# Kernel optimization log

Hardware: AMD Instinct MI355X
Metric: run time of the kernel (lower is better)

## Reference

```python
import jax, jax.numpy as jnp
import numpy as np

N, K, M = 1024, 256, 1024
INIT_SCALE = 0.1


def setup_inputs() -> dict:
    key = jax.random.key(0)
    kx, kw = jax.random.split(key)
    x = jax.random.normal(kx, (N, K), dtype=jnp.float32)
    weight = jax.random.normal(kw, (M, K), dtype=jnp.float32) * INIT_SCALE
    return {"x": x, "weight": weight}


def reference(x, weight):
    # Tropical (max-plus) matmul: out[n, m] = max_k(|x[n, k]| + |w[m, k]|)
    ax = jnp.abs(x)        # [N, K]
    aw = jnp.abs(weight)   # [M, K]
    # broadcast to [N, M, K] then reduce over K (mirrors the original expand+add+max)
    return jnp.max(ax[:, None, :] + aw[None, :, :], axis=2)  # [N, M]
```

## Files before the change

kernel.cpp:

```cpp
#include <hip/hip_runtime.h>


typedef float v2f __attribute__((ext_vector_type(2)));
typedef float v4f __attribute__((ext_vector_type(4)));

constexpr int K    = 256;
constexpr int N    = 1024;
constexpr int M    = 1024;
constexpr int TILE = 64;
constexpr int KH   = 128;
constexpr int KPL  = KH / 2;

__global__ void __launch_bounds__(256, 2)
tropical_main(const float* __restrict__ xg, const float* __restrict__ wg,
              float* __restrict__ pw)
{
    __shared__ __align__(16) v2f xs[KPL * 64];
    __shared__ __align__(16) v2f wsh[KPL * 64];

    const int tid = threadIdx.x;
    const int tx  = tid & 15;
    const int ty  = tid >> 4;
    const int bt  = (int)blockIdx.x & 255;
    const int kh  = (int)blockIdx.x >> 8;
    const int bn  = (bt >> 4) * TILE;
    const int bm  = (bt & 15) * TILE;
    const int k0  = kh * KH;

    const int r0 = tid >> 3;
    const int l  = tid & 7;
    const v4f* x0 = (const v4f*)(xg + (bn + r0     ) * K + k0);
    const v4f* x1 = (const v4f*)(xg + (bn + r0 + 32) * K + k0);
    const v4f* w0 = (const v4f*)(wg + (bm + r0     ) * K + k0);
    const v4f* w1 = (const v4f*)(wg + (bm + r0 + 32) * K + k0);

#pragma unroll
    for (int i = 0; i < 4; ++i) {
        const int q   = l + 8 * i;
        const int kpl = 2 * q;
        v4f a = x0[q];
        v4f b = x1[q];
        v4f c = w0[q];
        v4f d = w1[q];
        const int s0 = ((kpl    ) & 3) << 2;
        const int s1 = ((kpl + 1) & 3) << 2;
        xs [(kpl    ) * 64 + ((r0     ) ^ s0)] = (v2f){fabsf(a.x), fabsf(a.y)};
        xs [(kpl + 1) * 64 + ((r0     ) ^ s1)] = (v2f){fabsf(a.z), fabsf(a.w)};
        xs [(kpl    ) * 64 + ((r0 + 32) ^ s0)] = (v2f){fabsf(b.x), fabsf(b.y)};
        xs [(kpl + 1) * 64 + ((r0 + 32) ^ s1)] = (v2f){fabsf(b.z), fabsf(b.w)};
        wsh[(kpl    ) * 64 + ((r0     ) ^ s0)] = (v2f){fabsf(c.x), fabsf(c.y)};
        wsh[(kpl + 1) * 64 + ((r0     ) ^ s1)] = (v2f){fabsf(c.z), fabsf(c.w)};
        wsh[(kpl    ) * 64 + ((r0 + 32) ^ s0)] = (v2f){fabsf(d.x), fabsf(d.y)};
        wsh[(kpl + 1) * 64 + ((r0 + 32) ^ s1)] = (v2f){fabsf(d.z), fabsf(d.w)};
    }

    __syncthreads();

    float acc[4][4];
#pragma unroll
    for (int a2 = 0; a2 < 4; ++a2)
#pragma unroll
        for (int b2 = 0; b2 < 4; ++b2) acc[a2][b2] = 0.f;

    const int ty0 = ty;        const int tx0 = tx;
    const int ty4 = ty ^ 4;    const int tx4 = tx ^ 4;
    const int ty8 = ty ^ 8;    const int tx8 = tx ^ 8;
    const int ty12 = ty ^ 12;  const int tx12 = tx ^ 12;

#define PHASE(J, TYJ, TXJ)                                                   \
    do {                                                                     \
        const v2f* xr = xs  + (kp4 + (J)) * 64;                              \
        const v2f* wr = wsh + (kp4 + (J)) * 64;                              \
        v2f xa[4] = {xr[(TYJ)], xr[(TYJ) + 16], xr[(TYJ) + 32], xr[(TYJ) + 48]}; \
        v2f wa[4] = {wr[(TXJ)], wr[(TXJ) + 16], wr[(TXJ) + 32], wr[(TXJ) + 48]}; \
        _Pragma("unroll")                                                    \
        for (int a2 = 0; a2 < 4; ++a2)                                       \
            _Pragma("unroll")                                                \
            for (int b2 = 0; b2 < 4; ++b2) {                                 \
                v2f s = xa[a2] + wa[b2];                   \
                acc[a2][b2] = fmaxf(acc[a2][b2], fmaxf(s.x, s.y)); \
            }                                                                \
    } while (0)

    for (int kp4 = 0; kp4 < KPL; kp4 += 4) {
        PHASE(0, ty0,  tx0);
        PHASE(1, ty4,  tx4);
        PHASE(2, ty8,  tx8);
        PHASE(3, ty12, tx12);
    }
#undef PHASE

    float* slab = pw + kh * (N * M);
#pragma unroll
    for (int a2 = 0; a2 < 4; ++a2)
#pragma unroll
        for (int b2 = 0; b2 < 4; ++b2)
            slab[(bn + ty + 16 * a2) * M + (bm + tx + 16 * b2)] = acc[a2][b2];
}

__global__ void __launch_bounds__(256)
tropical_merge(const float* __restrict__ pw, float* __restrict__ outg)
{
    const int i = (int)blockIdx.x * 256 + (int)threadIdx.x;
    v4f a = ((const v4f*)pw)[i];
    v4f b = ((const v4f*)(pw + N * M))[i];
    v4f m = {fmaxf(a.x, b.x), fmaxf(a.y, b.y),
             fmaxf(a.z, b.z), fmaxf(a.w, b.w)};
    ((v4f*)outg)[i] = m;
}

extern "C" void kernel_launch(void* const* d_in, const int* in_sizes, int n_in,
                              void* d_out, int out_size, void* d_ws, size_t ws_size,
                              hipStream_t stream)
{
    const float* x = (const float*)d_in[0];
    const float* w = (const float*)d_in[1];
    float* out = (float*)d_out;
    float* ws  = (float*)d_ws;

    tropical_main<<<dim3(512), dim3(256), 0, stream>>>(x, w, ws);
    tropical_merge<<<dim3(N * M / 4 / 256), dim3(256), 0, stream>>>(ws, out);
}
```

Measured before the change: 75.75 us.

## Fuse split-K merge into main kernel via intra-block shared-memory reduction

The two K-halves are now computed by two groups of 256 threads inside one 512-thread block instead of two separate blocks. The halves are combined through shared memory, which removes the workspace slab writes, the second merge kernel launch, and its global reads. In exchange the grid shrinks from 512 to 256 blocks. Each block now needs twice the shared memory and adds two extra barriers.

```diff
diff --git a/kernel.cpp b/kernel.cpp
--- a/kernel.cpp
+++ b/kernel.cpp
@@ -8,53 +8,44 @@
 constexpr int N    = 1024;
 constexpr int M    = 1024;
 constexpr int TILE = 64;
-constexpr int KH   = 128;
-constexpr int KPL  = KH / 2;
+constexpr int KP   = K / 2;
 
-__global__ void __launch_bounds__(256, 2)
-tropical_main(const float* __restrict__ xg, const float* __restrict__ wg,
-              float* __restrict__ pw)
+__global__ void __launch_bounds__(512, 2)
+tropical_kernel(const float* __restrict__ xg, const float* __restrict__ wg,
+                float* __restrict__ outg)
 {
-    __shared__ __align__(16) v2f xs[KPL * 64];
-    __shared__ __align__(16) v2f wsh[KPL * 64];
+    __shared__ __align__(16) v2f xs[KP * 64];
+    __shared__ __align__(16) v2f wsh[KP * 64];
 
     const int tid = threadIdx.x;
-    const int tx  = tid & 15;
-    const int ty  = tid >> 4;
-    const int bt  = (int)blockIdx.x & 255;
-    const int kh  = (int)blockIdx.x >> 8;
-    const int bn  = (bt >> 4) * TILE;
-    const int bm  = (bt & 15) * TILE;
-    const int k0  = kh * KH;
+    const int bn  = (int)(blockIdx.x >> 4) * TILE;
+    const int bm  = (int)(blockIdx.x & 15) * TILE;
 
     const int r0 = tid >> 3;
     const int l  = tid & 7;
-    const v4f* x0 = (const v4f*)(xg + (bn + r0     ) * K + k0);
-    const v4f* x1 = (const v4f*)(xg + (bn + r0 + 32) * K + k0);
-    const v4f* w0 = (const v4f*)(wg + (bm + r0     ) * K + k0);
-    const v4f* w1 = (const v4f*)(wg + (bm + r0 + 32) * K + k0);
+    const float* xrow = xg + (bn + r0) * K;
+    const float* wrow = wg + (bm + r0) * K;
 
 #pragma unroll
-    for (int i = 0; i < 4; ++i) {
-        const int q   = l + 8 * i;
-        const int kpl = 2 * q;
-        v4f a = x0[q];
-        v4f b = x1[q];
-        v4f c = w0[q];
-        v4f d = w1[q];
-        const int s0 = ((kpl    ) & 3) << 2;
-        const int s1 = ((kpl + 1) & 3) << 2;
-        xs [(kpl    ) * 64 + ((r0     ) ^ s0)] = (v2f){fabsf(a.x), fabsf(a.y)};
-        xs [(kpl + 1) * 64 + ((r0     ) ^ s1)] = (v2f){fabsf(a.z), fabsf(a.w)};
-        xs [(kpl    ) * 64 + ((r0 + 32) ^ s0)] = (v2f){fabsf(b.x), fabsf(b.y)};
-        xs [(kpl + 1) * 64 + ((r0 + 32) ^ s1)] = (v2f){fabsf(b.z), fabsf(b.w)};
-        wsh[(kpl    ) * 64 + ((r0     ) ^ s0)] = (v2f){fabsf(c.x), fabsf(c.y)};
-        wsh[(kpl + 1) * 64 + ((r0     ) ^ s1)] = (v2f){fabsf(c.z), fabsf(c.w)};
-        wsh[(kpl    ) * 64 + ((r0 + 32) ^ s0)] = (v2f){fabsf(d.x), fabsf(d.y)};
-        wsh[(kpl + 1) * 64 + ((r0 + 32) ^ s1)] = (v2f){fabsf(d.z), fabsf(d.w)};
+    for (int i = 0; i < 8; ++i) {
+        const int q  = l + 8 * i;
+        const int kp = 2 * q;
+        v4f a = *(const v4f*)(xrow + 4 * q);
+        v4f c = *(const v4f*)(wrow + 4 * q);
+        const int s0 = ((kp    ) & 3) << 2;
+        const int s1 = ((kp + 1) & 3) << 2;
+        xs [(kp    ) * 64 + (r0 ^ s0)] = (v2f){fabsf(a.x), fabsf(a.y)};
+        xs [(kp + 1) * 64 + (r0 ^ s1)] = (v2f){fabsf(a.z), fabsf(a.w)};
+        wsh[(kp    ) * 64 + (r0 ^ s0)] = (v2f){fabsf(c.x), fabsf(c.y)};
+        wsh[(kp + 1) * 64 + (r0 ^ s1)] = (v2f){fabsf(c.z), fabsf(c.w)};
     }
 
     __syncthreads();
+
+    const int th   = tid & 255;
+    const int half = tid >> 8;
+    const int tx   = th & 15;
+    const int ty   = th >> 4;
 
     float acc[4][4];
 #pragma unroll
@@ -62,9 +53,9 @@
 #pragma unroll
         for (int b2 = 0; b2 < 4; ++b2) acc[a2][b2] = 0.f;
 
-    const int ty0 = ty;        const int tx0 = tx;
-    const int ty4 = ty ^ 4;    const int tx4 = tx ^ 4;
-    const int ty8 = ty ^ 8;    const int tx8 = tx ^ 8;
+    const int ty0  = ty;       const int tx0  = tx;
+    const int ty4  = ty ^ 4;   const int tx4  = tx ^ 4;
+    const int ty8  = ty ^ 8;   const int tx8  = tx ^ 8;
     const int ty12 = ty ^ 12;  const int tx12 = tx ^ 12;
 
 #define PHASE(J, TYJ, TXJ)                                                   \
@@ -82,7 +73,8 @@
             }                                                                \
     } while (0)
 
-    for (int kp4 = 0; kp4 < KPL; kp4 += 4) {
+    const int kbeg = half * 64;
+    for (int kp4 = kbeg; kp4 < kbeg + 64; kp4 += 4) {
         PHASE(0, ty0,  tx0);
         PHASE(1, ty4,  tx4);
         PHASE(2, ty8,  tx8);
@@ -90,23 +82,30 @@
     }
 #undef PHASE
 
-    float* slab = pw + kh * (N * M);
+    __syncthreads();
+    v4f* mb = (v4f*)xs;
+    if (half == 1) {
 #pragma unroll
-    for (int a2 = 0; a2 < 4; ++a2)
+        for (int a2 = 0; a2 < 4; ++a2)
+            mb[a2 * 256 + th] =
+                (v4f){acc[a2][0], acc[a2][1], acc[a2][2], acc[a2][3]};
+    }
+    __syncthreads();
+    if (half == 0) {
 #pragma unroll
-        for (int b2 = 0; b2 < 4; ++b2)
-            slab[(bn + ty + 16 * a2) * M + (bm + tx + 16 * b2)] = acc[a2][b2];
-}
-
-__global__ void __launch_bounds__(256)
-tropical_merge(const float* __restrict__ pw, float* __restrict__ outg)
-{
-    const int i = (int)blockIdx.x * 256 + (int)threadIdx.x;
-    v4f a = ((const v4f*)pw)[i];
-    v4f b = ((const v4f*)(pw + N * M))[i];
-    v4f m = {fmaxf(a.x, b.x), fmaxf(a.y, b.y),
-             fmaxf(a.z, b.z), fmaxf(a.w, b.w)};
-    ((v4f*)outg)[i] = m;
+        for (int a2 = 0; a2 < 4; ++a2) {
+            v4f o = mb[a2 * 256 + th];
+            float m0 = fmaxf(acc[a2][0], o.x);
+            float m1 = fmaxf(acc[a2][1], o.y);
+            float m2 = fmaxf(acc[a2][2], o.z);
+            float m3 = fmaxf(acc[a2][3], o.w);
+            float* orow = outg + (bn + ty + 16 * a2) * M + bm;
+            orow[tx     ] = m0;
+            orow[tx + 16] = m1;
+            orow[tx + 32] = m2;
+            orow[tx + 48] = m3;
+        }
+    }
 }
 
 extern "C" void kernel_launch(void* const* d_in, const int* in_sizes, int n_in,
@@ -116,8 +115,8 @@
     const float* x = (const float*)d_in[0];
     const float* w = (const float*)d_in[1];
     float* out = (float*)d_out;
-    float* ws  = (float*)d_ws;
 
-    tropical_main<<<dim3(512), dim3(256), 0, stream>>>(x, w, ws);
-    tropical_merge<<<dim3(N * M / 4 / 256), dim3(256), 0, stream>>>(ws, out);
+    dim3 grid(256);
+    dim3 block(512);
+    tropical_kernel<<<grid, block, 0, stream>>>(x, w, out);
 }
```

Measured after the change: 71.59 us. 1.06x faster.
